# Performance work log

Hardware: AMD Instinct MI355X
Metric: run time of the kernel (lower is better)

The kernel has to match this reference:

```python
import jax, jax.numpy as jnp
import numpy as np

B, S, D, H = 2, 2048, 1024, 16
HD = D // H


def setup_inputs() -> dict:
    key = jax.random.key(0)
    ks = jax.random.split(key, 8)
    std = 1.0 / np.sqrt(D)
    return {
        "q": jax.random.normal(ks[0], (B, S, D), jnp.float32),
        "k": jax.random.normal(ks[1], (B, S, D), jnp.float32),
        "v": jax.random.normal(ks[2], (B, S, D), jnp.float32),
        "mask": jnp.ones((B, S, S), jnp.int32),
        "Wq": jax.random.normal(ks[3], (D, D), jnp.float32) * std,
        "bq": jax.random.normal(ks[4], (D,), jnp.float32) * std,
        "Wout": jax.random.normal(ks[5], (D, D), jnp.float32) * std,
        "bout": jax.random.normal(ks[6], (D,), jnp.float32) * std,
    }


def _split_heads(x):
    # [B, S, D] -> [B, H, S, HD]
    b, s, _ = x.shape
    return x.reshape(b, s, H, HD).transpose(0, 2, 1, 3)


def reference(q, k, v, mask, Wq, bq, Wout, bout):
    # NOTE: source module uses q_linear for q, k AND v (faithful reproduction)
    qp = _split_heads(q @ Wq.T + bq)
    kp = _split_heads(k @ Wq.T + bq)
    vp = _split_heads(v @ Wq.T + bq)
    scale = 1.0 / jnp.sqrt(jnp.float32(HD))
    scores = jnp.einsum("bhqd,bhkd->bhqk", qp, kp) * scale  # [B,H,S,S]
    m = mask[:, None, :, :]  # [B,1,S,S]
    scores = jnp.where(m == 0, jnp.float32(-1e9), scores)
    attn_weights = jax.nn.softmax(scores, axis=-1)
    ctx = jnp.einsum("bhqk,bhkd->bhqd", attn_weights, vp)
    out = ctx.transpose(0, 2, 1, 3).reshape(q.shape[0], q.shape[1], D)
    out = out @ Wout.T + bout
    return out, attn_weights
```

## Files before the change

### kernel.cpp

```cpp
#include <hip/hip_runtime.h>
#include <hip/hip_bf16.h>
#include <stdint.h>

typedef float    f32x4 __attribute__((ext_vector_type(4)));
typedef __bf16   bf16x8 __attribute__((ext_vector_type(8)));
typedef uint16_t u16;
typedef uint16_t u16x8 __attribute__((ext_vector_type(8)));
typedef uint16_t u16x4 __attribute__((ext_vector_type(4)));

__device__ __forceinline__ u16 f2bf(float f) {
  uint32_t u = __builtin_bit_cast(uint32_t, f);
  u += 0x7fffu + ((u >> 16) & 1u);
  return (u16)(u >> 16);
}

__device__ __forceinline__ f32x4 mfma16(u16x8 a, u16x8 b, f32x4 c) {
  return __builtin_amdgcn_mfma_f32_16x16x32_bf16(
      __builtin_bit_cast(bf16x8, a), __builtin_bit_cast(bf16x8, b), c, 0, 0, 0);
}

__global__ void conv_kernel(const float* __restrict__ src, u16* __restrict__ dst, int n4) {
  int i = blockIdx.x * blockDim.x + threadIdx.x;
  if (i >= n4) return;
  f32x4 v = *(const f32x4*)(src + (size_t)i * 4);
  u16x4 o;
  #pragma unroll
  for (int j = 0; j < 4; ++j) o[j] = f2bf(v[j]);
  *(u16x4*)(dst + (size_t)i * 4) = o;
}

__global__ void maskpack_kernel(const int* __restrict__ mask,
                                unsigned long long* __restrict__ bits) {
  int t = blockIdx.x * 256 + threadIdx.x;
  int mv = __builtin_nontemporal_load(mask + t);
  unsigned long long bal = __ballot(mv != 0);
  if ((threadIdx.x & 63) == 0) bits[t >> 6] = bal;
}

__global__ __launch_bounds__(256) void proj_kernel(
    const float* __restrict__ qin, const float* __restrict__ kin,
    const float* __restrict__ vin, const u16* __restrict__ wb,
    const float* __restrict__ bias,
    u16* __restrict__ qp, u16* __restrict__ kp, u16* __restrict__ vpt) {
  __shared__ __attribute__((aligned(16))) u16 lds_a[128][72];
  __shared__ __attribute__((aligned(16))) u16 lds_b[128][72];
  const int tid = threadIdx.x;
  const int lane = tid & 63, wv = tid >> 6;
  const int wr = wv >> 1, wc = wv & 1;
  const int g = lane >> 4, li = lane & 15;
  const int nb = blockIdx.x, mb = blockIdx.y, src = blockIdx.z;
  const float* A = (src == 0) ? qin : (src == 1) ? kin : vin;

  const int arow = tid >> 1;
  const int acol = (tid & 1) * 32;

  f32x4 acc[4][4];
  #pragma unroll
  for (int m = 0; m < 4; ++m)
    #pragma unroll
    for (int n = 0; n < 4; ++n) acc[m][n] = f32x4{0.f, 0.f, 0.f, 0.f};

  const float* aptr = A + (size_t)(mb * 128 + arow) * 1024 + acol;
  const u16*   bptr = wb + (size_t)(nb * 128 + arow) * 1024 + acol;

  for (int kt = 0; kt < 16; ++kt) {
    f32x4 af[8];
    #pragma unroll
    for (int i = 0; i < 8; ++i) af[i] = *(const f32x4*)(aptr + kt * 64 + i * 4);
    #pragma unroll
    for (int i = 0; i < 4; ++i) {
      u16x8 p;
      #pragma unroll
      for (int j = 0; j < 8; ++j) p[j] = f2bf(af[i * 2 + (j >> 2)][j & 3]);
      *(u16x8*)&lds_a[arow][acol + i * 8] = p;
    }
    #pragma unroll
    for (int i = 0; i < 4; ++i)
      *(u16x8*)&lds_b[arow][acol + i * 8] = *(const u16x8*)(bptr + kt * 64 + i * 8);
    __syncthreads();
    #pragma unroll
    for (int kk = 0; kk < 2; ++kk) {
      const int kof = kk * 32 + g * 8;
      u16x8 afr[4], bfr[4];
      #pragma unroll
      for (int m = 0; m < 4; ++m) afr[m] = *(const u16x8*)&lds_a[wr * 64 + m * 16 + li][kof];
      #pragma unroll
      for (int n = 0; n < 4; ++n) bfr[n] = *(const u16x8*)&lds_b[wc * 64 + n * 16 + li][kof];
      #pragma unroll
      for (int m = 0; m < 4; ++m)
        #pragma unroll
        for (int n = 0; n < 4; ++n) acc[m][n] = mfma16(afr[m], bfr[n], acc[m][n]);
    }
    __syncthreads();
  }

  #pragma unroll
  for (int n = 0; n < 4; ++n) {
    const int col = nb * 128 + wc * 64 + n * 16 + li;
    const float bv = bias[col];
    const int h = col >> 6, hd = col & 63;
    #pragma unroll
    for (int m = 0; m < 4; ++m) {
      const int row0 = mb * 128 + wr * 64 + m * 16 + g * 4;
      const int bb = row0 >> 11, s0 = row0 & 2047;
      if (src < 2) {
        u16* dst = (src == 0) ? qp : kp;
        #pragma unroll
        for (int r = 0; r < 4; ++r)
          dst[(((size_t)bb * 16 + h) * 2048 + s0 + r) * 64 + hd] = f2bf(acc[m][n][r] + bv);
      } else {
        u16x4 p;
        #pragma unroll
        for (int r = 0; r < 4; ++r) p[r] = f2bf(acc[m][n][r] + bv);
        *(u16x4*)&vpt[(((size_t)bb * 16 + h) * 64 + hd) * 2048 + s0] = p;
      }
    }
  }
}

__global__ __launch_bounds__(256) void attn_kernel(
    const u16* __restrict__ qp, const u16* __restrict__ kp,
    const u16* __restrict__ vpt, const unsigned long long* __restrict__ mbits,
    float* __restrict__ attnw, u16* __restrict__ ctx) {
  __shared__ __attribute__((aligned(16))) u16 q_lds[64][72];
  __shared__ __attribute__((aligned(16))) u16 k_lds[64][72];
  __shared__ __attribute__((aligned(16))) u16 v_lds[64][72];
  __shared__ __attribute__((aligned(16))) u16 w_lds[64][72];
  __shared__ unsigned long long m_lds[64][32];

  const int tid = threadIdx.x;
  const int lane = tid & 63, wv = tid >> 6;
  const int g = lane >> 4, li = lane & 15;
  const int qt = blockIdx.x, h = blockIdx.y, b = blockIdx.z;
  const int bh = b * 16 + h;
  const int q0 = qt * 64;
  const float scale = 0.125f;

  const int srow = tid >> 2;
  const int scol = (tid & 3) * 16;

  {
    const u16* qsrc = qp + ((size_t)bh * 2048 + q0 + srow) * 64 + scol;
    *(u16x8*)&q_lds[srow][scol] = *(const u16x8*)qsrc;
    *(u16x8*)&q_lds[srow][scol + 8] = *(const u16x8*)(qsrc + 8);
    const int mw0 = (tid & 3) * 8;
    #pragma unroll
    for (int i = 0; i < 8; ++i)
      m_lds[srow][mw0 + i] = mbits[((size_t)b * 2048 + q0 + srow) * 32 + mw0 + i];
  }
  __syncthreads();

  float mrun[4], lrun[4];
  #pragma unroll
  for (int r = 0; r < 4; ++r) { mrun[r] = -1e30f; lrun[r] = 0.f; }

  for (int kt = 0; kt < 32; ++kt) {
    const u16* ksrc = kp + ((size_t)bh * 2048 + kt * 64 + srow) * 64 + scol;
    *(u16x8*)&k_lds[srow][scol] = *(const u16x8*)ksrc;
    *(u16x8*)&k_lds[srow][scol + 8] = *(const u16x8*)(ksrc + 8);
    __syncthreads();
    f32x4 sc[4];
    #pragma unroll
    for (int n = 0; n < 4; ++n) sc[n] = f32x4{0.f, 0.f, 0.f, 0.f};
    #pragma unroll
    for (int kk = 0; kk < 2; ++kk) {
      const int kof = kk * 32 + g * 8;
      u16x8 aq = *(const u16x8*)&q_lds[wv * 16 + li][kof];
      #pragma unroll
      for (int n = 0; n < 4; ++n)
        sc[n] = mfma16(aq, *(const u16x8*)&k_lds[n * 16 + li][kof], sc[n]);
    }
    #pragma unroll
    for (int r = 0; r < 4; ++r) {
      const unsigned long long mw = m_lds[wv * 16 + g * 4 + r][kt];
      float pm = -1e30f;
      #pragma unroll
      for (int n = 0; n < 4; ++n) {
        float sv = ((mw >> (n * 16 + li)) & 1ull) ? sc[n][r] * scale : -1e9f;
        sc[n][r] = sv;
        pm = fmaxf(pm, sv);
      }
      #pragma unroll
      for (int off = 1; off < 16; off <<= 1) pm = fmaxf(pm, __shfl_xor(pm, off, 16));
      const float mnew = fmaxf(mrun[r], pm);
      float ps = 0.f;
      #pragma unroll
      for (int n = 0; n < 4; ++n) ps += __expf(sc[n][r] - mnew);
      #pragma unroll
      for (int off = 1; off < 16; off <<= 1) ps += __shfl_xor(ps, off, 16);
      lrun[r] = lrun[r] * __expf(mrun[r] - mnew) + ps;
      mrun[r] = mnew;
    }
    __syncthreads();
  }

  float inv[4];
  #pragma unroll
  for (int r = 0; r < 4; ++r) inv[r] = 1.f / lrun[r];

  f32x4 cacc[4];
  #pragma unroll
  for (int n = 0; n < 4; ++n) cacc[n] = f32x4{0.f, 0.f, 0.f, 0.f};

  for (int kt = 0; kt < 32; ++kt) {
    const u16* ksrc = kp + ((size_t)bh * 2048 + kt * 64 + srow) * 64 + scol;
    *(u16x8*)&k_lds[srow][scol] = *(const u16x8*)ksrc;
    *(u16x8*)&k_lds[srow][scol + 8] = *(const u16x8*)(ksrc + 8);
    const u16* vsrc = vpt + ((size_t)bh * 64 + srow) * 2048 + kt * 64 + scol;
    *(u16x8*)&v_lds[srow][scol] = *(const u16x8*)vsrc;
    *(u16x8*)&v_lds[srow][scol + 8] = *(const u16x8*)(vsrc + 8);
    __syncthreads();
    f32x4 sc[4];
    #pragma unroll
    for (int n = 0; n < 4; ++n) sc[n] = f32x4{0.f, 0.f, 0.f, 0.f};
    #pragma unroll
    for (int kk = 0; kk < 2; ++kk) {
      const int kof = kk * 32 + g * 8;
      u16x8 aq = *(const u16x8*)&q_lds[wv * 16 + li][kof];
      #pragma unroll
      for (int n = 0; n < 4; ++n)
        sc[n] = mfma16(aq, *(const u16x8*)&k_lds[n * 16 + li][kof], sc[n]);
    }
    #pragma unroll
    for (int r = 0; r < 4; ++r) {
      const int row_l = wv * 16 + g * 4 + r;
      const unsigned long long mw = m_lds[row_l][kt];
      float* wdst = attnw + ((size_t)bh * 2048 + q0 + row_l) * 2048 + kt * 64;
      #pragma unroll
      for (int n = 0; n < 4; ++n) {
        float sv = ((mw >> (n * 16 + li)) & 1ull) ? sc[n][r] * scale : -1e9f;
        float wn = __expf(sv - mrun[r]) * inv[r];
        __builtin_nontemporal_store(wn, wdst + n * 16 + li);
        w_lds[row_l][n * 16 + li] = f2bf(wn);
      }
    }
    __syncthreads();
    #pragma unroll
    for (int kk = 0; kk < 2; ++kk) {
      const int kof = kk * 32 + g * 8;
      u16x8 aw = *(const u16x8*)&w_lds[wv * 16 + li][kof];
      #pragma unroll
      for (int n = 0; n < 4; ++n)
        cacc[n] = mfma16(aw, *(const u16x8*)&v_lds[n * 16 + li][kof], cacc[n]);
    }
    __syncthreads();
  }

  #pragma unroll
  for (int n = 0; n < 4; ++n)
    #pragma unroll
    for (int r = 0; r < 4; ++r) {
      const int row_l = wv * 16 + g * 4 + r;
      ctx[((size_t)b * 2048 + q0 + row_l) * 1024 + h * 64 + n * 16 + li] = f2bf(cacc[n][r]);
    }
}

__global__ __launch_bounds__(256) void out_kernel(
    const u16* __restrict__ ctxp, const u16* __restrict__ wb,
    const float* __restrict__ bias, float* __restrict__ out) {
  __shared__ __attribute__((aligned(16))) u16 lds_a[128][72];
  __shared__ __attribute__((aligned(16))) u16 lds_b[128][72];
  const int tid = threadIdx.x;
  const int lane = tid & 63, wv = tid >> 6;
  const int wr = wv >> 1, wc = wv & 1;
  const int g = lane >> 4, li = lane & 15;
  const int nb = blockIdx.x, mb = blockIdx.y;

  const int arow = tid >> 1;
  const int acol = (tid & 1) * 32;

  f32x4 acc[4][4];
  #pragma unroll
  for (int m = 0; m < 4; ++m)
    #pragma unroll
    for (int n = 0; n < 4; ++n) acc[m][n] = f32x4{0.f, 0.f, 0.f, 0.f};

  const u16* aptr = ctxp + (size_t)(mb * 128 + arow) * 1024 + acol;
  const u16* bptr = wb + (size_t)(nb * 128 + arow) * 1024 + acol;

  for (int kt = 0; kt < 16; ++kt) {
    #pragma unroll
    for (int i = 0; i < 4; ++i) {
      *(u16x8*)&lds_a[arow][acol + i * 8] = *(const u16x8*)(aptr + kt * 64 + i * 8);
      *(u16x8*)&lds_b[arow][acol + i * 8] = *(const u16x8*)(bptr + kt * 64 + i * 8);
    }
    __syncthreads();
    #pragma unroll
    for (int kk = 0; kk < 2; ++kk) {
      const int kof = kk * 32 + g * 8;
      u16x8 afr[4], bfr[4];
      #pragma unroll
      for (int m = 0; m < 4; ++m) afr[m] = *(const u16x8*)&lds_a[wr * 64 + m * 16 + li][kof];
      #pragma unroll
      for (int n = 0; n < 4; ++n) bfr[n] = *(const u16x8*)&lds_b[wc * 64 + n * 16 + li][kof];
      #pragma unroll
      for (int m = 0; m < 4; ++m)
        #pragma unroll
        for (int n = 0; n < 4; ++n) acc[m][n] = mfma16(afr[m], bfr[n], acc[m][n]);
    }
    __syncthreads();
  }

  #pragma unroll
  for (int n = 0; n < 4; ++n) {
    const int col = nb * 128 + wc * 64 + n * 16 + li;
    const float bv = bias[col];
    #pragma unroll
    for (int m = 0; m < 4; ++m) {
      const int row0 = mb * 128 + wr * 64 + m * 16 + g * 4;
      #pragma unroll
      for (int r = 0; r < 4; ++r)
        __builtin_nontemporal_store(acc[m][n][r] + bv, out + (size_t)(row0 + r) * 1024 + col);
    }
  }
}

extern "C" void kernel_launch(void* const* d_in, const int* in_sizes, int n_in,
                              void* d_out, int out_size, void* d_ws, size_t ws_size,
                              hipStream_t stream) {
  const float* q    = (const float*)d_in[0];
  const float* k    = (const float*)d_in[1];
  const float* v    = (const float*)d_in[2];
  const int*   mask = (const int*)d_in[3];
  const float* Wq   = (const float*)d_in[4];
  const float* bq   = (const float*)d_in[5];
  const float* Wout = (const float*)d_in[6];
  const float* bout = (const float*)d_in[7];
  float* out   = (float*)d_out;
  float* attnw = out + (size_t)2 * 2048 * 1024;

  u16* wq_bf   = (u16*)d_ws;
  u16* wout_bf = wq_bf + (1 << 20);
  u16* qp      = wout_bf + (1 << 20);
  u16* kp      = qp + (4 << 20);
  u16* vpt     = kp + (4 << 20);
  u16* ctx     = vpt + (4 << 20);
  unsigned long long* mbits = (unsigned long long*)(ctx + (4 << 20));

  conv_kernel<<<1024, 256, 0, stream>>>(Wq, wq_bf, 262144);
  conv_kernel<<<1024, 256, 0, stream>>>(Wout, wout_bf, 262144);
  maskpack_kernel<<<32768, 256, 0, stream>>>(mask, mbits);
  proj_kernel<<<dim3(8, 32, 3), 256, 0, stream>>>(q, k, v, wq_bf, bq, qp, kp, vpt);
  attn_kernel<<<dim3(32, 16, 2), 256, 0, stream>>>(qp, kp, vpt, mbits, attnw, ctx);
  out_kernel<<<dim3(8, 32), 256, 0, stream>>>(ctx, wout_bf, bout, out);
}
```

Before: 846.2 us.

## Pre-convert QKV to bf16, register-prefetch tiles, defer softmax row reductions

Adds a separate kernel that converts q/k/v to bf16 once, so the projection GEMM loads bf16 and no longer converts fp32 inside its loop. The projection, attention and output GEMMs now prefetch the next K/V/A/B tile into registers while the current tile is being computed, which overlaps global loads with MFMA work. The attention first pass keeps per-lane running max and sum and merges them across the 16 lanes only once at the end, removing shuffles from every tile. One barrier in the second pass is dropped. In exchange there is an extra launch with a 24 MB bf16 staging round trip, and register pressure rises.

```diff
diff --git a/kernel.cpp b/kernel.cpp
--- a/kernel.cpp
+++ b/kernel.cpp
@@ -7,6 +7,7 @@
 typedef uint16_t u16;
 typedef uint16_t u16x8 __attribute__((ext_vector_type(8)));
 typedef uint16_t u16x4 __attribute__((ext_vector_type(4)));
+typedef unsigned long long u64;
 
 __device__ __forceinline__ u16 f2bf(float f) {
   uint32_t u = __builtin_bit_cast(uint32_t, f);
@@ -29,17 +30,30 @@
   *(u16x4*)(dst + (size_t)i * 4) = o;
 }
 
+__global__ void convqkv_kernel(const float* __restrict__ q, const float* __restrict__ k,
+                               const float* __restrict__ v, u16* __restrict__ xb) {
+  int t = blockIdx.x * 256 + threadIdx.x;
+  int src = t >> 19;
+  size_t off = (size_t)(t & 524287) * 8;
+  const float* p = ((src == 0) ? q : (src == 1) ? k : v) + off;
+  f32x4 a = *(const f32x4*)p;
+  f32x4 b = *(const f32x4*)(p + 4);
+  u16x8 o;
+  #pragma unroll
+  for (int j = 0; j < 4; ++j) { o[j] = f2bf(a[j]); o[4 + j] = f2bf(b[j]); }
+  *(u16x8*)(xb + (size_t)t * 8) = o;
+}
+
 __global__ void maskpack_kernel(const int* __restrict__ mask,
-                                unsigned long long* __restrict__ bits) {
+                                u64* __restrict__ bits) {
   int t = blockIdx.x * 256 + threadIdx.x;
   int mv = __builtin_nontemporal_load(mask + t);
-  unsigned long long bal = __ballot(mv != 0);
+  u64 bal = __ballot(mv != 0);
   if ((threadIdx.x & 63) == 0) bits[t >> 6] = bal;
 }
 
 __global__ __launch_bounds__(256) void proj_kernel(
-    const float* __restrict__ qin, const float* __restrict__ kin,
-    const float* __restrict__ vin, const u16* __restrict__ wb,
+    const u16* __restrict__ xb, const u16* __restrict__ wb,
     const float* __restrict__ bias,
     u16* __restrict__ qp, u16* __restrict__ kp, u16* __restrict__ vpt) {
   __shared__ __attribute__((aligned(16))) u16 lds_a[128][72];
@@ -48,9 +62,7 @@
   const int lane = tid & 63, wv = tid >> 6;
   const int wr = wv >> 1, wc = wv & 1;
   const int g = lane >> 4, li = lane & 15;
-  const int nb = blockIdx.x, mb = blockIdx.y, src = blockIdx.z;
-  const float* A = (src == 0) ? qin : (src == 1) ? kin : vin;
-
+  const int nb = blockIdx.x, mb = blockIdx.y;
   const int arow = tid >> 1;
   const int acol = (tid & 1) * 32;
 
@@ -60,23 +72,29 @@
     #pragma unroll
     for (int n = 0; n < 4; ++n) acc[m][n] = f32x4{0.f, 0.f, 0.f, 0.f};
 
-  const float* aptr = A + (size_t)(mb * 128 + arow) * 1024 + acol;
-  const u16*   bptr = wb + (size_t)(nb * 128 + arow) * 1024 + acol;
+  const u16* aptr = xb + (size_t)(mb * 128 + arow) * 1024 + acol;
+  const u16* bptr = wb + (size_t)(nb * 128 + arow) * 1024 + acol;
+
+  u16x8 ar[4], br[4];
+  #pragma unroll
+  for (int i = 0; i < 4; ++i) {
+    ar[i] = *(const u16x8*)(aptr + i * 8);
+    br[i] = *(const u16x8*)(bptr + i * 8);
+  }
 
   for (int kt = 0; kt < 16; ++kt) {
-    f32x4 af[8];
-    #pragma unroll
-    for (int i = 0; i < 8; ++i) af[i] = *(const f32x4*)(aptr + kt * 64 + i * 4);
     #pragma unroll
     for (int i = 0; i < 4; ++i) {
-      u16x8 p;
-      #pragma unroll
-      for (int j = 0; j < 8; ++j) p[j] = f2bf(af[i * 2 + (j >> 2)][j & 3]);
-      *(u16x8*)&lds_a[arow][acol + i * 8] = p;
-    }
-    #pragma unroll
-    for (int i = 0; i < 4; ++i)
-      *(u16x8*)&lds_b[arow][acol + i * 8] = *(const u16x8*)(bptr + kt * 64 + i * 8);
+      *(u16x8*)&lds_a[arow][acol + i * 8] = ar[i];
+      *(u16x8*)&lds_b[arow][acol + i * 8] = br[i];
+    }
+    if (kt < 15) {
+      #pragma unroll
+      for (int i = 0; i < 4; ++i) {
+        ar[i] = *(const u16x8*)(aptr + (kt + 1) * 64 + i * 8);
+        br[i] = *(const u16x8*)(bptr + (kt + 1) * 64 + i * 8);
+      }
+    }
     __syncthreads();
     #pragma unroll
     for (int kk = 0; kk < 2; ++kk) {
@@ -101,8 +119,9 @@
     const int h = col >> 6, hd = col & 63;
     #pragma unroll
     for (int m = 0; m < 4; ++m) {
-      const int row0 = mb * 128 + wr * 64 + m * 16 + g * 4;
-      const int bb = row0 >> 11, s0 = row0 & 2047;
+      const int tok0 = mb * 128 + wr * 64 + m * 16 + g * 4;
+      const int src = tok0 >> 12;
+      const int bb = (tok0 >> 11) & 1, s0 = tok0 & 2047;
       if (src < 2) {
         u16* dst = (src == 0) ? qp : kp;
         #pragma unroll
@@ -120,13 +139,13 @@
 
 __global__ __launch_bounds__(256) void attn_kernel(
     const u16* __restrict__ qp, const u16* __restrict__ kp,
-    const u16* __restrict__ vpt, const unsigned long long* __restrict__ mbits,
+    const u16* __restrict__ vpt, const u64* __restrict__ mbits,
     float* __restrict__ attnw, u16* __restrict__ ctx) {
   __shared__ __attribute__((aligned(16))) u16 q_lds[64][72];
   __shared__ __attribute__((aligned(16))) u16 k_lds[64][72];
   __shared__ __attribute__((aligned(16))) u16 v_lds[64][72];
   __shared__ __attribute__((aligned(16))) u16 w_lds[64][72];
-  __shared__ unsigned long long m_lds[64][32];
+  __shared__ u64 m_lds[64][32];
 
   const int tid = threadIdx.x;
   const int lane = tid & 63, wv = tid >> 6;
@@ -135,9 +154,12 @@
   const int bh = b * 16 + h;
   const int q0 = qt * 64;
   const float scale = 0.125f;
-
   const int srow = tid >> 2;
   const int scol = (tid & 3) * 16;
+
+  const u16* kbase = kp + ((size_t)bh * 2048 + srow) * 64 + scol;
+  u16x8 k0 = *(const u16x8*)kbase;
+  u16x8 k1 = *(const u16x8*)(kbase + 8);
 
   {
     const u16* qsrc = qp + ((size_t)bh * 2048 + q0 + srow) * 64 + scol;
@@ -148,16 +170,20 @@
     for (int i = 0; i < 8; ++i)
       m_lds[srow][mw0 + i] = mbits[((size_t)b * 2048 + q0 + srow) * 32 + mw0 + i];
   }
+
+  float mlane[4], llane[4];
+  #pragma unroll
+  for (int r = 0; r < 4; ++r) { mlane[r] = -1e30f; llane[r] = 0.f; }
+
   __syncthreads();
 
-  float mrun[4], lrun[4];
-  #pragma unroll
-  for (int r = 0; r < 4; ++r) { mrun[r] = -1e30f; lrun[r] = 0.f; }
-
   for (int kt = 0; kt < 32; ++kt) {
-    const u16* ksrc = kp + ((size_t)bh * 2048 + kt * 64 + srow) * 64 + scol;
-    *(u16x8*)&k_lds[srow][scol] = *(const u16x8*)ksrc;
-    *(u16x8*)&k_lds[srow][scol + 8] = *(const u16x8*)(ksrc + 8);
+    *(u16x8*)&k_lds[srow][scol] = k0;
+    *(u16x8*)&k_lds[srow][scol + 8] = k1;
+    if (kt < 31) {
+      k0 = *(const u16x8*)(kbase + (size_t)(kt + 1) * 4096);
+      k1 = *(const u16x8*)(kbase + (size_t)(kt + 1) * 4096 + 8);
+    }
     __syncthreads();
     f32x4 sc[4];
     #pragma unroll
@@ -172,43 +198,58 @@
     }
     #pragma unroll
     for (int r = 0; r < 4; ++r) {
-      const unsigned long long mw = m_lds[wv * 16 + g * 4 + r][kt];
-      float pm = -1e30f;
-      #pragma unroll
-      for (int n = 0; n < 4; ++n) {
-        float sv = ((mw >> (n * 16 + li)) & 1ull) ? sc[n][r] * scale : -1e9f;
-        sc[n][r] = sv;
-        pm = fmaxf(pm, sv);
-      }
-      #pragma unroll
-      for (int off = 1; off < 16; off <<= 1) pm = fmaxf(pm, __shfl_xor(pm, off, 16));
-      const float mnew = fmaxf(mrun[r], pm);
-      float ps = 0.f;
-      #pragma unroll
-      for (int n = 0; n < 4; ++n) ps += __expf(sc[n][r] - mnew);
-      #pragma unroll
-      for (int off = 1; off < 16; off <<= 1) ps += __shfl_xor(ps, off, 16);
-      lrun[r] = lrun[r] * __expf(mrun[r] - mnew) + ps;
-      mrun[r] = mnew;
-    }
-    __syncthreads();
-  }
-
-  float inv[4];
-  #pragma unroll
-  for (int r = 0; r < 4; ++r) inv[r] = 1.f / lrun[r];
+      const u64 mw = m_lds[wv * 16 + g * 4 + r][kt];
+      float sv[4];
+      #pragma unroll
+      for (int n = 0; n < 4; ++n)
+        sv[n] = ((mw >> (n * 16 + li)) & 1ull) ? sc[n][r] * scale : -1e9f;
+      float pm = fmaxf(fmaxf(sv[0], sv[1]), fmaxf(sv[2], sv[3]));
+      float mn = fmaxf(mlane[r], pm);
+      float ps = __expf(sv[0] - mn) + __expf(sv[1] - mn) +
+                 __expf(sv[2] - mn) + __expf(sv[3] - mn);
+      llane[r] = llane[r] * __expf(mlane[r] - mn) + ps;
+      mlane[r] = mn;
+    }
+    __syncthreads();
+  }
+
+  float mrow[4], inv[4];
+  #pragma unroll
+  for (int r = 0; r < 4; ++r) {
+    float m = mlane[r], l = llane[r];
+    #pragma unroll
+    for (int off = 1; off < 16; off <<= 1) {
+      float mo = __shfl_xor(m, off, 16);
+      float lo = __shfl_xor(l, off, 16);
+      float mn = fmaxf(m, mo);
+      l = l * __expf(m - mn) + lo * __expf(mo - mn);
+      m = mn;
+    }
+    mrow[r] = m;
+    inv[r] = 1.f / l;
+  }
+
+  const u16* vbase = vpt + ((size_t)bh * 64 + srow) * 2048 + scol;
+  k0 = *(const u16x8*)kbase;
+  k1 = *(const u16x8*)(kbase + 8);
+  u16x8 v0 = *(const u16x8*)vbase;
+  u16x8 v1 = *(const u16x8*)(vbase + 8);
 
   f32x4 cacc[4];
   #pragma unroll
   for (int n = 0; n < 4; ++n) cacc[n] = f32x4{0.f, 0.f, 0.f, 0.f};
 
   for (int kt = 0; kt < 32; ++kt) {
-    const u16* ksrc = kp + ((size_t)bh * 2048 + kt * 64 + srow) * 64 + scol;
-    *(u16x8*)&k_lds[srow][scol] = *(const u16x8*)ksrc;
-    *(u16x8*)&k_lds[srow][scol + 8] = *(const u16x8*)(ksrc + 8);
-    const u16* vsrc = vpt + ((size_t)bh * 64 + srow) * 2048 + kt * 64 + scol;
-    *(u16x8*)&v_lds[srow][scol] = *(const u16x8*)vsrc;
-    *(u16x8*)&v_lds[srow][scol + 8] = *(const u16x8*)(vsrc + 8);
+    *(u16x8*)&k_lds[srow][scol] = k0;
+    *(u16x8*)&k_lds[srow][scol + 8] = k1;
+    *(u16x8*)&v_lds[srow][scol] = v0;
+    *(u16x8*)&v_lds[srow][scol + 8] = v1;
+    if (kt < 31) {
+      k0 = *(const u16x8*)(kbase + (size_t)(kt + 1) * 4096);
+      k1 = *(const u16x8*)(kbase + (size_t)(kt + 1) * 4096 + 8);
+      v0 = *(const u16x8*)(vbase + (size_t)(kt + 1) * 64);
+      v1 = *(const u16x8*)(vbase + (size_t)(kt + 1) * 64 + 8);
+    }
     __syncthreads();
     f32x4 sc[4];
     #pragma unroll
@@ -224,17 +265,16 @@
     #pragma unroll
     for (int r = 0; r < 4; ++r) {
       const int row_l = wv * 16 + g * 4 + r;
-      const unsigned long long mw = m_lds[row_l][kt];
+      const u64 mw = m_lds[row_l][kt];
       float* wdst = attnw + ((size_t)bh * 2048 + q0 + row_l) * 2048 + kt * 64;
       #pragma unroll
       for (int n = 0; n < 4; ++n) {
         float sv = ((mw >> (n * 16 + li)) & 1ull) ? sc[n][r] * scale : -1e9f;
-        float wn = __expf(sv - mrun[r]) * inv[r];
+        float wn = __expf(sv - mrow[r]) * inv[r];
         __builtin_nontemporal_store(wn, wdst + n * 16 + li);
         w_lds[row_l][n * 16 + li] = f2bf(wn);
       }
     }
-    __syncthreads();
     #pragma unroll
     for (int kk = 0; kk < 2; ++kk) {
       const int kof = kk * 32 + g * 8;
@@ -265,7 +305,6 @@
   const int wr = wv >> 1, wc = wv & 1;
   const int g = lane >> 4, li = lane & 15;
   const int nb = blockIdx.x, mb = blockIdx.y;
-
   const int arow = tid >> 1;
   const int acol = (tid & 1) * 32;
 
@@ -278,11 +317,25 @@
   const u16* aptr = ctxp + (size_t)(mb * 128 + arow) * 1024 + acol;
   const u16* bptr = wb + (size_t)(nb * 128 + arow) * 1024 + acol;
 
+  u16x8 ar[4], br[4];
+  #pragma unroll
+  for (int i = 0; i < 4; ++i) {
+    ar[i] = *(const u16x8*)(aptr + i * 8);
+    br[i] = *(const u16x8*)(bptr + i * 8);
+  }
+
   for (int kt = 0; kt < 16; ++kt) {
     #pragma unroll
     for (int i = 0; i < 4; ++i) {
-      *(u16x8*)&lds_a[arow][acol + i * 8] = *(const u16x8*)(aptr + kt * 64 + i * 8);
-      *(u16x8*)&lds_b[arow][acol + i * 8] = *(const u16x8*)(bptr + kt * 64 + i * 8);
+      *(u16x8*)&lds_a[arow][acol + i * 8] = ar[i];
+      *(u16x8*)&lds_b[arow][acol + i * 8] = br[i];
+    }
+    if (kt < 15) {
+      #pragma unroll
+      for (int i = 0; i < 4; ++i) {
+        ar[i] = *(const u16x8*)(aptr + (kt + 1) * 64 + i * 8);
+        br[i] = *(const u16x8*)(bptr + (kt + 1) * 64 + i * 8);
+      }
     }
     __syncthreads();
     #pragma unroll
@@ -329,18 +382,21 @@
   float* out   = (float*)d_out;
   float* attnw = out + (size_t)2 * 2048 * 1024;
 
-  u16* wq_bf   = (u16*)d_ws;
-  u16* wout_bf = wq_bf + (1 << 20);
-  u16* qp      = wout_bf + (1 << 20);
-  u16* kp      = qp + (4 << 20);
-  u16* vpt     = kp + (4 << 20);
-  u16* ctx     = vpt + (4 << 20);
-  unsigned long long* mbits = (unsigned long long*)(ctx + (4 << 20));
+  u16* ws16    = (u16*)d_ws;
+  u16* wq_bf   = ws16;
+  u16* wout_bf = ws16 + 1048576;
+  u16* xb      = ws16 + 2097152;
+  u16* qp      = ws16 + 14680064;
+  u16* kp      = ws16 + 18874368;
+  u16* vpt     = ws16 + 23068672;
+  u16* ctx     = ws16 + 27262976;
+  u64* mbits   = (u64*)(ws16 + 31457280);
 
   conv_kernel<<<1024, 256, 0, stream>>>(Wq, wq_bf, 262144);
   conv_kernel<<<1024, 256, 0, stream>>>(Wout, wout_bf, 262144);
+  convqkv_kernel<<<6144, 256, 0, stream>>>(q, k, v, xb);
   maskpack_kernel<<<32768, 256, 0, stream>>>(mask, mbits);
-  proj_kernel<<<dim3(8, 32, 3), 256, 0, stream>>>(q, k, v, wq_bf, bq, qp, kp, vpt);
+  proj_kernel<<<dim3(8, 96), 256, 0, stream>>>(xb, wq_bf, bq, qp, kp, vpt);
   attn_kernel<<<dim3(32, 16, 2), 256, 0, stream>>>(qp, kp, vpt, mbits, attnw, ctx);
   out_kernel<<<dim3(8, 32), 256, 0, stream>>>(ctx, wout_bf, bout, out);
 }
```

Measured after the change: 784.8 us. -7.3%, faster.
